# Performance work log

Hardware: AMD Instinct MI355X
Metric: run time of the kernel (lower is better)

The kernel has to match this reference:

```python
import jax, jax.numpy as jnp
from jax import lax
import numpy as np

D_MODEL, D_STATE, D_CONV, D_INNER = 1024, 16, 4, 2048
BATCH, SEQ = 2, 2048


def setup_inputs() -> dict:
    key = jax.random.key(0)
    ks = jax.random.split(key, 7)
    s = lambda fan: 1.0 / np.sqrt(fan)
    return {
        "x": jax.random.normal(ks[0], (BATCH, SEQ, D_MODEL), jnp.float32),
        "W_in": jax.random.normal(ks[1], (2 * D_INNER, D_MODEL), jnp.float32) * s(D_MODEL),
        "conv_w": jax.random.normal(ks[2], (D_INNER, 1, D_CONV), jnp.float32) * s(D_CONV),
        "conv_b": jax.random.normal(ks[3], (D_INNER,), jnp.float32) * 0.02,
        "A_log": jax.random.normal(ks[4], (D_INNER, D_STATE), jnp.float32),
        "W_x": jax.random.normal(ks[5], (2 * D_STATE + 1, D_INNER), jnp.float32) * s(D_INNER),
        "W_out": jax.random.normal(ks[6], (D_MODEL, D_INNER), jnp.float32) * s(D_INNER),
    }


def reference(x, W_in, conv_w, conv_b, A_log, W_x, W_out):
    B, L, _ = x.shape
    di, ds = D_INNER, D_STATE

    # in_proj and chunk into (x_proj, z)
    xz = jnp.einsum("bld,ed->ble", x, W_in)          # [B, L, 2*di]
    xp, z = xz[..., :di], xz[..., di:]

    # depthwise causal conv1d: padding = d_conv-1 on left, then trim to L
    xc = jnp.transpose(xp, (0, 2, 1))                 # [B, di, L]
    xc = lax.conv_general_dilated(
        xc, conv_w, window_strides=(1,), padding=[(D_CONV - 1, 0)],
        feature_group_count=di)
    xc = xc + conv_b[None, :, None]
    xc = jnp.transpose(xc, (0, 2, 1))                 # [B, L, di]
    xc = jax.nn.silu(xc)

    A = -jnp.exp(A_log.astype(jnp.float32))           # [di, ds]

    # input-dependent delta, B, C
    xdbl = jnp.einsum("bld,ed->ble", xc, W_x)         # [B, L, 2*ds+1]
    delta = jax.nn.softplus(xdbl[..., :1])            # [B, L, 1]
    Bm = xdbl[..., 1:1 + ds]                          # [B, L, ds]
    Cm = xdbl[..., 1 + ds:]                           # [B, L, ds]

    # selective scan: h_t = exp(delta_t * A) * h_{t-1} + delta_t * B_t (outer) u_t
    def step(h, inp):
        d_t, b_t, c_t, u_t = inp                      # [B,1], [B,ds], [B,ds], [B,di]
        dA = jnp.exp(d_t[:, :, None] * A[None])       # [B, di, ds]
        h = dA * h + d_t[:, :, None] * b_t[:, None, :] * u_t[:, :, None]
        y_t = jnp.einsum("bds,bs->bd", h, c_t)        # [B, di]
        return h, y_t

    h0 = jnp.zeros((B, di, ds), xc.dtype)
    inps = (jnp.swapaxes(delta, 0, 1), jnp.swapaxes(Bm, 0, 1),
            jnp.swapaxes(Cm, 0, 1), jnp.swapaxes(xc, 0, 1))
    _, ys = lax.scan(step, h0, inps)                  # ys: [L, B, di]
    y = jnp.swapaxes(ys, 0, 1)                        # [B, L, di]

    y = y * jax.nn.silu(z)
    return jnp.einsum("bld,ed->ble", y, W_out)        # [B, L, d_model]
```

## Files before the change

kernel.cpp:

```cpp
#include <hip/hip_runtime.h>

#define DM    1024
#define DS    16
#define DI    2048
#define LSEQ  2048
#define BL    4096
#define NC    128
#define CHK   16

typedef float          f32x4  __attribute__((ext_vector_type(4)));
typedef float          f32x16 __attribute__((ext_vector_type(16)));
typedef unsigned int   u32x4  __attribute__((ext_vector_type(4)));
typedef unsigned short u16x8  __attribute__((ext_vector_type(8)));

__device__ __forceinline__ unsigned short f2bf(float f) {
    unsigned int u = __float_as_uint(f);
    u += 0x7fffu + ((u >> 16) & 1u);
    return (unsigned short)(u >> 16);
}

__device__ __forceinline__ float bf2f(unsigned short u) {
    return __uint_as_float((unsigned int)u << 16);
}

__device__ __forceinline__ float silu_f(float x) {
    return x / (1.f + __expf(-x));
}

__device__ __forceinline__ void mfma_bf16(f32x4& d, const u32x4& a, const u32x4& b) {
    asm("v_mfma_f32_16x16x32_bf16 %0, %1, %2, %0" : "+v"(d) : "v"(a), "v"(b));
}

__device__ __forceinline__ void gload16(const void* g, void* l) {
    __builtin_amdgcn_global_load_lds(
        (const __attribute__((address_space(1))) unsigned int*)g,
        (__attribute__((address_space(3))) unsigned int*)l, 16, 0, 0);
}

__global__ __launch_bounds__(256) void prep_inputs_kernel(const float* __restrict__ x,
                                                          const float* __restrict__ W_in,
                                                          unsigned short* __restrict__ xbf,
                                                          unsigned short* __restrict__ wbf) {
    const int n4 = (BL * DM) / 4;
    int i = blockIdx.x * 256 + threadIdx.x;
    const float* src = (i < n4) ? x : W_in;
    unsigned short* dst = (i < n4) ? xbf : wbf;
    int j = (i < n4) ? i : i - n4;
    float4 v = *(const float4*)(src + j * 4);
    ushort4 o;
    o.x = f2bf(v.x); o.y = f2bf(v.y); o.z = f2bf(v.z); o.w = f2bf(v.w);
    *(ushort4*)(dst + j * 4) = o;
}

__global__ __launch_bounds__(256) void prep_weights_kernel(const float* __restrict__ W_out,
                                                           const float* __restrict__ Wx,
                                                           unsigned short* __restrict__ wobf,
                                                           unsigned short* __restrict__ wxbf) {
    const int n4 = (DM * DI) / 4;
    int i = blockIdx.x * 256 + threadIdx.x;
    if (i < n4) {
        float4 v = *(const float4*)(W_out + i * 4);
        ushort4 o;
        o.x = f2bf(v.x); o.y = f2bf(v.y); o.z = f2bf(v.z); o.w = f2bf(v.w);
        *(ushort4*)(wobf + i * 4) = o;
    } else {
        int j = i - n4;
        if (j < 128 * 2048) {
            int e = j >> 11;
            wxbf[j] = (e < 33) ? f2bf(Wx[j]) : (unsigned short)0;
        }
    }
}

template <typename OUT>
__global__ __launch_bounds__(512, 2) void gemm256_bf16_nt(const unsigned short* __restrict__ A,
                                                          const unsigned short* __restrict__ B,
                                                          OUT* __restrict__ C,
                                                          int M, int N, int K) {
    __shared__ unsigned short As[4][256 * 32];
    __shared__ unsigned short Bs[4][256 * 32];

    const int tid  = threadIdx.x;
    const int lane = tid & 63;
    const int wave = tid >> 6;
    const int wm = wave >> 2;
    const int wn = wave & 3;
    const int lrow = lane & 15, lkh = lane >> 4;
    const int swa  = (lrow >> 1) & 3;

    const long m0 = (long)blockIdx.y * 256;
    const long n0 = (long)blockIdx.x * 256;

    const int scb = ((tid & 3) ^ ((tid >> 3) & 3)) * 8;
    const unsigned short* pa = A + (m0 + (tid >> 2)) * K + scb;
    const unsigned short* pb = B + (n0 + (tid >> 2)) * K + scb;
    const long rstep = (long)128 * K;

    const int NT = K >> 5;

    f32x4 acc[8][4];
#pragma unroll
    for (int i = 0; i < 8; ++i)
#pragma unroll
        for (int j = 0; j < 4; ++j)
            acc[i][j] = (f32x4){0.f, 0.f, 0.f, 0.f};

#define STAGE_A(t) { char* d_ = (char*)&As[(t) & 3][0] + wave * 1024;          \
                     gload16(pa + (long)(t) * 32,         d_);                 \
                     gload16(pa + rstep + (long)(t) * 32, d_ + 8192); }
#define STAGE_B(t) { char* d_ = (char*)&Bs[(t) & 3][0] + wave * 1024;          \
                     gload16(pb + (long)(t) * 32,         d_);                 \
                     gload16(pb + rstep + (long)(t) * 32, d_ + 8192); }

    STAGE_A(0); STAGE_B(0);
    STAGE_A(1); STAGE_B(1);
    STAGE_A(2); STAGE_B(2);
    asm volatile("s_waitcnt vmcnt(8)" ::: "memory");
    __builtin_amdgcn_s_barrier();
    __builtin_amdgcn_sched_barrier(0);

    for (int t = 0; t < NT; ++t) {
        const unsigned short* as = &As[t & 3][0];
        const unsigned short* bs = &Bs[t & 3][0];
        const bool st = (t + 3 < NT);

        u32x4 af[4], bfr[4];
#pragma unroll
        for (int j = 0; j < 4; ++j)
            bfr[j] = *(const u32x4*)(bs + (wn * 64 + j * 16 + lrow) * 32 + ((lkh ^ swa) * 8));
#pragma unroll
        for (int i = 0; i < 4; ++i)
            af[i] = *(const u32x4*)(as + (wm * 128 + i * 16 + lrow) * 32 + ((lkh ^ swa) * 8));
        if (st) STAGE_A(t + 3);
        asm volatile("s_waitcnt lgkmcnt(0)" ::: "memory");
        __builtin_amdgcn_sched_barrier(0);
        __builtin_amdgcn_s_setprio(1);
#pragma unroll
        for (int i = 0; i < 4; ++i)
#pragma unroll
            for (int j = 0; j < 4; ++j)
                mfma_bf16(acc[i][j], af[i], bfr[j]);
        __builtin_amdgcn_s_setprio(0);

#pragma unroll
        for (int i = 0; i < 4; ++i)
            af[i] = *(const u32x4*)(as + (wm * 128 + (i + 4) * 16 + lrow) * 32 + ((lkh ^ swa) * 8));
        if (st) STAGE_B(t + 3);
        asm volatile("s_waitcnt lgkmcnt(0)" ::: "memory");
        __builtin_amdgcn_sched_barrier(0);
        __builtin_amdgcn_s_setprio(1);
#pragma unroll
        for (int i = 0; i < 4; ++i)
#pragma unroll
            for (int j = 0; j < 4; ++j)
                mfma_bf16(acc[i + 4][j], af[i], bfr[j]);
        __builtin_amdgcn_s_setprio(0);

        if (t < NT - 1) {
            if (t <= NT - 4)      asm volatile("s_waitcnt vmcnt(8)" ::: "memory");
            else if (t == NT - 3) asm volatile("s_waitcnt vmcnt(4)" ::: "memory");
            else                  asm volatile("s_waitcnt vmcnt(0)" ::: "memory");
            __builtin_amdgcn_s_barrier();
            __builtin_amdgcn_sched_barrier(0);
        }
    }
#undef STAGE_A
#undef STAGE_B

    asm volatile("s_nop 7\n\ts_nop 7" ::: "memory");

#pragma unroll
    for (int i = 0; i < 8; ++i)
#pragma unroll
        for (int j = 0; j < 4; ++j)
#pragma unroll
            for (int r = 0; r < 4; ++r) {
                long row = m0 + wm * 128 + i * 16 + lkh * 4 + r;
                long col = n0 + wn * 64 + j * 16 + lrow;
                float v = acc[i][j][r];
                if constexpr (sizeof(OUT) == 2) C[row * (long)N + col] = f2bf(v);
                else                            C[row * (long)N + col] = v;
            }
}

template <int NF, typename OUT>
__global__ __launch_bounds__(256) void gemm_bf16_nt(const unsigned short* __restrict__ A,
                                                    const unsigned short* __restrict__ B,
                                                    OUT* __restrict__ C,
                                                    int M, int N, int K, int KS) {
    constexpr int BN = NF * 32;
    __shared__ unsigned short As[2][128 * 32];
    __shared__ unsigned short Bs[2][BN * 32];

    const int tid  = threadIdx.x;
    const int lane = tid & 63;
    const int wave = tid >> 6;
    const int wr = wave >> 1, wc = wave & 1;
    const int lrow = lane & 15, lkh = lane >> 4;

    const long m0 = (long)blockIdx.y * 128;
    const long n0 = (long)blockIdx.x * BN;
    const int koff = blockIdx.z * KS;

    const int scb = ((tid & 3) ^ ((tid >> 3) & 3)) * 8;
    const unsigned short* pa = A + (m0 + (tid >> 2)) * K + koff + scb;
    const unsigned short* pb = B + (n0 + (tid >> 2)) * K + koff + scb;
    const long half = (long)64 * K;

    OUT* Cz = C + (long)blockIdx.z * M * (long)N;

    const int swa = (lrow >> 1) & 3;

    f32x4 acc[4][NF];
#pragma unroll
    for (int i = 0; i < 4; ++i)
#pragma unroll
        for (int j = 0; j < NF; ++j)
            acc[i][j] = (f32x4){0.f, 0.f, 0.f, 0.f};

    auto STAGE = [&](int buf, int k0) {
        char* a = (char*)&As[buf][0] + wave * 1024;
        gload16(pa + k0,        a);
        gload16(pa + half + k0, a + 4096);
        char* b = (char*)&Bs[buf][0] + wave * 1024;
        gload16(pb + k0, b);
        if constexpr (NF == 4) gload16(pb + half + k0, b + 4096);
    };

    STAGE(0, 0);
    asm volatile("s_waitcnt vmcnt(0)" ::: "memory");
    __builtin_amdgcn_s_barrier();
    __builtin_amdgcn_sched_barrier(0);

    int cur = 0;
    for (int k0 = 0; k0 < KS; k0 += 32) {
        const bool notlast = (k0 + 32 < KS);
        if (notlast) STAGE(cur ^ 1, k0 + 32);

        u32x4 af[4], bfr[NF];
#pragma unroll
        for (int i = 0; i < 4; ++i)
            af[i] = *(const u32x4*)(&As[cur][(wr * 64 + i * 16 + lrow) * 32 + ((lkh ^ swa) * 8)]);
#pragma unroll
        for (int j = 0; j < NF; ++j)
            bfr[j] = *(const u32x4*)(&Bs[cur][(wc * NF * 16 + j * 16 + lrow) * 32 + ((lkh ^ swa) * 8)]);

        __builtin_amdgcn_s_setprio(1);
#pragma unroll
        for (int i = 0; i < 4; ++i)
#pragma unroll
            for (int j = 0; j < NF; ++j)
                mfma_bf16(acc[i][j], af[i], bfr[j]);
        __builtin_amdgcn_s_setprio(0);

        if (notlast) {
            asm volatile("s_waitcnt vmcnt(0)" ::: "memory");
            __builtin_amdgcn_s_barrier();
            __builtin_amdgcn_sched_barrier(0);
            cur ^= 1;
        }
    }

    asm volatile("s_nop 7\n\ts_nop 7" ::: "memory");

#pragma unroll
    for (int i = 0; i < 4; ++i)
#pragma unroll
        for (int j = 0; j < NF; ++j)
#pragma unroll
            for (int r = 0; r < 4; ++r) {
                long row = m0 + wr * 64 + i * 16 + lkh * 4 + r;
                long col = n0 + wc * NF * 16 + j * 16 + lrow;
                float v = acc[i][j][r];
                if constexpr (sizeof(OUT) == 2) Cz[row * (long)N + col] = f2bf(v);
                else                            Cz[row * (long)N + col] = v;
            }
}

__global__ __launch_bounds__(256) void conv_silu_kernel(const unsigned short* __restrict__ xzbf,
                                                        const float* __restrict__ cw,
                                                        const float* __restrict__ cb,
                                                        unsigned short* __restrict__ xcbf) {
    int idx = blockIdx.x * 256 + threadIdx.x;
    int d8 = (idx & 255) * 8;
    int m  = idx >> 8;
    int t  = m & (LSEQ - 1);
    const unsigned short* p = xzbf + (long)m * (2 * DI) + d8;
    u16x8 tap0 = (u16x8)(0), tap1 = (u16x8)(0), tap2 = (u16x8)(0);
    u16x8 tap3 = *(const u16x8*)(p);
    if (t >= 1) tap2 = *(const u16x8*)(p - 1 * 2 * DI);
    if (t >= 2) tap1 = *(const u16x8*)(p - 2 * 2 * DI);
    if (t >= 3) tap0 = *(const u16x8*)(p - 3 * 2 * DI);

    u16x8 o;
#pragma unroll
    for (int k = 0; k < 8; ++k) {
        const float4 wv = *(const float4*)(cw + 4 * (d8 + k));
        float s = cb[d8 + k];
        s = fmaf(bf2f(tap0[k]), wv.x, s);
        s = fmaf(bf2f(tap1[k]), wv.y, s);
        s = fmaf(bf2f(tap2[k]), wv.z, s);
        s = fmaf(bf2f(tap3[k]), wv.w, s);
        o[k] = f2bf(silu_f(s));
    }
    *(u16x8*)(xcbf + (long)m * DI + d8) = o;
}

__global__ __launch_bounds__(256) void xdbl_reduce_kernel(const float* __restrict__ part,
                                                          float* __restrict__ dlt,
                                                          float* __restrict__ BC) {
    int idx = blockIdx.x * 256 + threadIdx.x;
    if (idx >= BL * 33) return;
    int m = idx / 33;
    int j = idx - m * 33;
    float v = 0.f;
#pragma unroll
    for (int g = 0; g < 8; ++g) v += part[(long)g * (BL * 128) + (long)m * 128 + j];
    if (j == 0) dlt[m] = (v > 20.f) ? v : log1pf(expf(v));
    else        BC[(long)m * 32 + (j - 1)] = v;
}

__global__ __launch_bounds__(256, 4) void scan_pass1(const float* __restrict__ dlt,
                                                     const float* __restrict__ BC,
                                                     const unsigned short* __restrict__ xcbf,
                                                     const float* __restrict__ A_log,
                                                     float* __restrict__ P_,
                                                     float* __restrict__ S_) {
    __shared__ float sdl[CHK];
    __shared__ float sbc[CHK * 32];

    const int tid = threadIdx.x;
    const int c   = blockIdx.x;
    const int ch  = blockIdx.y * 256 + tid;
    const int b   = ch >> 11;
    const int d   = ch & (DI - 1);
    const long m0 = (long)b * LSEQ + (long)c * CHK;

    if (tid < CHK * 8) *(float4*)(sbc + tid * 4) = *(const float4*)(BC + m0 * 32 + tid * 4);
    if (tid < CHK) sdl[tid] = dlt[m0 + tid];

    f32x16 A2, h;
#pragma unroll
    for (int s = 0; s < 16; ++s) {
        A2[s] = -__expf(A_log[d * 16 + s]) * 1.44269504f;
        h[s] = 0.f;
    }
    const unsigned short* ur = xcbf + m0 * DI + d;
    float sumdl = 0.f;
    __syncthreads();

#pragma unroll
    for (int t0 = 0; t0 < CHK; t0 += 4) {
        float uu[4], dd[4];
#pragma unroll
        for (int k = 0; k < 4; ++k) {
            uu[k] = bf2f(ur[(long)(t0 + k) * DI]);
            dd[k] = sdl[t0 + k];
        }
#pragma unroll
        for (int k = 0; k < 4; ++k) {
            const int t = t0 + k;
            float dl = dd[k];
            float du = dl * uu[k];
            sumdl += dl;
#pragma unroll
            for (int q = 0; q < 4; ++q) {
                f32x4 bq = *(const f32x4*)(sbc + t * 32 + q * 4);
#pragma unroll
                for (int j = 0; j < 4; ++j) {
                    const int s = q * 4 + j;
                    float dA = exp2f(dl * A2[s]);
                    h[s] = fmaf(dA, h[s], du * bq[j]);
                }
            }
        }
    }
    float* pp = P_ + ((long)c * 4096 + ch) * 16;
    float* sp = S_ + ((long)c * 4096 + ch) * 16;
#pragma unroll
    for (int q = 0; q < 4; ++q) {
        f32x4 pv;
#pragma unroll
        for (int j = 0; j < 4; ++j) pv[j] = exp2f(A2[q * 4 + j] * sumdl);
        *(f32x4*)(pp + q * 4) = pv;
        *(f32x4*)(sp + q * 4) = (f32x4){h[q*4], h[q*4+1], h[q*4+2], h[q*4+3]};
    }
}

__global__ __launch_bounds__(256) void scan_pass2(const float* __restrict__ P_,
                                                  float* __restrict__ S_) {
    const long idx = (long)blockIdx.x * 256 + threadIdx.x;
    float h = 0.f;
    for (int c0 = 0; c0 < NC; c0 += 8) {
        float p[8], s[8];
#pragma unroll
        for (int i = 0; i < 8; ++i) {
            p[i] = P_[(long)(c0 + i) * 65536 + idx];
            s[i] = S_[(long)(c0 + i) * 65536 + idx];
        }
#pragma unroll
        for (int i = 0; i < 8; ++i) {
            S_[(long)(c0 + i) * 65536 + idx] = h;
            h = fmaf(p[i], h, s[i]);
        }
    }
}

__global__ __launch_bounds__(256, 4) void scan_pass3(const float* __restrict__ dlt,
                                                     const float* __restrict__ BC,
                                                     const unsigned short* __restrict__ xcbf,
                                                     const unsigned short* __restrict__ xzbf,
                                                     const float* __restrict__ A_log,
                                                     const float* __restrict__ H0,
                                                     unsigned short* __restrict__ ybf) {
    __shared__ float sdl[CHK];
    __shared__ float sbc[CHK * 32];

    const int tid = threadIdx.x;
    const int c   = blockIdx.x;
    const int ch  = blockIdx.y * 256 + tid;
    const int b   = ch >> 11;
    const int d   = ch & (DI - 1);
    const long m0 = (long)b * LSEQ + (long)c * CHK;

    if (tid < CHK * 8) *(float4*)(sbc + tid * 4) = *(const float4*)(BC + m0 * 32 + tid * 4);
    if (tid < CHK) sdl[tid] = dlt[m0 + tid];

    f32x16 A2, h;
    const float* h0p = H0 + ((long)c * 4096 + ch) * 16;
    {
        f32x4 h0a = *(const f32x4*)(h0p + 0);
        f32x4 h0b = *(const f32x4*)(h0p + 4);
        f32x4 h0c = *(const f32x4*)(h0p + 8);
        f32x4 h0d = *(const f32x4*)(h0p + 12);
#pragma unroll
        for (int j = 0; j < 4; ++j) {
            h[j]      = h0a[j];
            h[4 + j]  = h0b[j];
            h[8 + j]  = h0c[j];
            h[12 + j] = h0d[j];
        }
    }
#pragma unroll
    for (int s = 0; s < 16; ++s) A2[s] = -__expf(A_log[d * 16 + s]) * 1.44269504f;

    const unsigned short* ur = xcbf + m0 * DI + d;
    const unsigned short* zr = xzbf + m0 * (2 * DI) + DI + d;
    unsigned short* yr = ybf + m0 * DI + d;
    __syncthreads();

#pragma unroll
    for (int t0 = 0; t0 < CHK; t0 += 4) {
        float uu[4], zz[4], dd[4];
#pragma unroll
        for (int k = 0; k < 4; ++k) {
            uu[k] = bf2f(ur[(long)(t0 + k) * DI]);
            zz[k] = bf2f(zr[(long)(t0 + k) * 2 * DI]);
            dd[k] = sdl[t0 + k];
        }
#pragma unroll
        for (int k = 0; k < 4; ++k) {
            const int t = t0 + k;
            float dl = dd[k];
            float du = dl * uu[k];
            f32x4 yv = (f32x4){0.f, 0.f, 0.f, 0.f};
#pragma unroll
            for (int q = 0; q < 4; ++q) {
                f32x4 bq = *(const f32x4*)(sbc + t * 32 + q * 4);
                f32x4 cq = *(const f32x4*)(sbc + t * 32 + 16 + q * 4);
#pragma unroll
                for (int j = 0; j < 4; ++j) {
                    const int s = q * 4 + j;
                    float dA = exp2f(dl * A2[s]);
                    h[s] = fmaf(dA, h[s], du * bq[j]);
                    yv[q] = fmaf(h[s], cq[j], yv[q]);
                }
            }
            float y = (yv[0] + yv[1]) + (yv[2] + yv[3]);
            yr[(long)t * DI] = f2bf(y * silu_f(zz[k]));
        }
    }
}

extern "C" void kernel_launch(void* const* d_in, const int* in_sizes, int n_in,
                              void* d_out, int out_size, void* d_ws, size_t ws_size,
                              hipStream_t stream) {
    const float* x      = (const float*)d_in[0];
    const float* W_in   = (const float*)d_in[1];
    const float* conv_w = (const float*)d_in[2];
    const float* conv_b = (const float*)d_in[3];
    const float* A_log  = (const float*)d_in[4];
    const float* W_x    = (const float*)d_in[5];
    const float* W_out  = (const float*)d_in[6];
    float* out = (float*)d_out;

    char* w = (char*)d_ws;
    unsigned short* xbf  = (unsigned short*)(w + 0);
    unsigned short* wbf  = (unsigned short*)(w + 8388608);
    unsigned short* xzbf = (unsigned short*)(w + 16777216);
    unsigned short* xcbf = (unsigned short*)(w + 50331648);
    float*          dlt  = (float*)(w + 67108864);
    float*          BC   = (float*)(w + 67125248);
    float*          P_   = (float*)(w + 67649536);
    float*          S_   = (float*)(w + 101203968);

    unsigned short* wobf      = xbf;
    unsigned short* wxbf      = (unsigned short*)(w + 8388608);
    float*          xdbl_part = (float*)P_;
    unsigned short* ybf       = (unsigned short*)P_;

    prep_inputs_kernel<<<dim3(8192), dim3(256), 0, stream>>>(x, W_in, xbf, wbf);
    gemm256_bf16_nt<unsigned short><<<dim3(16, 16), dim3(512), 0, stream>>>(xbf, wbf, xzbf, BL, 2 * DI, DM);
    prep_weights_kernel<<<dim3(3072), dim3(256), 0, stream>>>(W_out, W_x, wobf, wxbf);
    conv_silu_kernel<<<dim3((BL * DI / 8) / 256), dim3(256), 0, stream>>>(xzbf, conv_w, conv_b, xcbf);
    gemm_bf16_nt<4, float><<<dim3(1, 32, 8), dim3(256), 0, stream>>>(xcbf, wxbf, xdbl_part, BL, 128, DI, 256);
    xdbl_reduce_kernel<<<dim3(528), dim3(256), 0, stream>>>(xdbl_part, dlt, BC);
    scan_pass1<<<dim3(NC, 16), dim3(256), 0, stream>>>(dlt, BC, xcbf, A_log, P_, S_);
    scan_pass2<<<dim3(256), dim3(256), 0, stream>>>(P_, S_);
    scan_pass3<<<dim3(NC, 16), dim3(256), 0, stream>>>(dlt, BC, xcbf, xzbf, A_log, S_, ybf);
    gemm_bf16_nt<2, float><<<dim3(16, 32, 1), dim3(256), 0, stream>>>(ybf, wobf, out, BL, DM, DI, DI);
}
```

Before: 229.6 us.

## Precompute A2 in prep kernel, double scan chunk size, drop scan LDS staging

```diff
diff --git a/kernel.cpp b/kernel.cpp
--- a/kernel.cpp
+++ b/kernel.cpp
@@ -5,13 +5,19 @@
 #define DI    2048
 #define LSEQ  2048
 #define BL    4096
-#define NC    128
-#define CHK   16
+#define NC    64
+#define CHK   32
 
 typedef float          f32x4  __attribute__((ext_vector_type(4)));
 typedef float          f32x16 __attribute__((ext_vector_type(16)));
 typedef unsigned int   u32x4  __attribute__((ext_vector_type(4)));
 typedef unsigned short u16x8  __attribute__((ext_vector_type(8)));
+
+#if __has_builtin(__builtin_amdgcn_exp2f)
+#define EXP2(x) __builtin_amdgcn_exp2f(x)
+#else
+#define EXP2(x) __expf((x) * 0.6931471805599453f)
+#endif
 
 __device__ __forceinline__ unsigned short f2bf(float f) {
     unsigned int u = __float_as_uint(f);
@@ -54,8 +60,10 @@
 
 __global__ __launch_bounds__(256) void prep_weights_kernel(const float* __restrict__ W_out,
                                                            const float* __restrict__ Wx,
+                                                           const float* __restrict__ A_log,
                                                            unsigned short* __restrict__ wobf,
-                                                           unsigned short* __restrict__ wxbf) {
+                                                           unsigned short* __restrict__ wxbf,
+                                                           float* __restrict__ A2) {
     const int n4 = (DM * DI) / 4;
     int i = blockIdx.x * 256 + threadIdx.x;
     if (i < n4) {
@@ -68,6 +76,9 @@
         if (j < 128 * 2048) {
             int e = j >> 11;
             wxbf[j] = (e < 33) ? f2bf(Wx[j]) : (unsigned short)0;
+        } else {
+            int k = j - 128 * 2048;
+            if (k < DI * DS) A2[k] = -__expf(A_log[k]) * 1.44269504f;
         }
     }
 }
@@ -320,15 +331,12 @@
     else        BC[(long)m * 32 + (j - 1)] = v;
 }
 
-__global__ __launch_bounds__(256, 4) void scan_pass1(const float* __restrict__ dlt,
-                                                     const float* __restrict__ BC,
-                                                     const unsigned short* __restrict__ xcbf,
-                                                     const float* __restrict__ A_log,
-                                                     float* __restrict__ P_,
-                                                     float* __restrict__ S_) {
-    __shared__ float sdl[CHK];
-    __shared__ float sbc[CHK * 32];
-
+__global__ __launch_bounds__(256) void scan_pass1(const float* __restrict__ dlt,
+                                                  const float* __restrict__ BC,
+                                                  const unsigned short* __restrict__ xcbf,
+                                                  const float* __restrict__ A2t,
+                                                  float* __restrict__ P_,
+                                                  float* __restrict__ S_) {
     const int tid = threadIdx.x;
     const int c   = blockIdx.x;
     const int ch  = blockIdx.y * 256 + tid;
@@ -336,40 +344,42 @@
     const int d   = ch & (DI - 1);
     const long m0 = (long)b * LSEQ + (long)c * CHK;
 
-    if (tid < CHK * 8) *(float4*)(sbc + tid * 4) = *(const float4*)(BC + m0 * 32 + tid * 4);
-    if (tid < CHK) sdl[tid] = dlt[m0 + tid];
-
     f32x16 A2, h;
-#pragma unroll
-    for (int s = 0; s < 16; ++s) {
-        A2[s] = -__expf(A_log[d * 16 + s]) * 1.44269504f;
-        h[s] = 0.f;
+    {
+        const float* ap = A2t + d * 16;
+        f32x4 a0 = *(const f32x4*)(ap + 0);
+        f32x4 a1 = *(const f32x4*)(ap + 4);
+        f32x4 a2 = *(const f32x4*)(ap + 8);
+        f32x4 a3 = *(const f32x4*)(ap + 12);
+#pragma unroll
+        for (int j = 0; j < 4; ++j) {
+            A2[j] = a0[j]; A2[4 + j] = a1[j]; A2[8 + j] = a2[j]; A2[12 + j] = a3[j];
+            h[j] = 0.f; h[4 + j] = 0.f; h[8 + j] = 0.f; h[12 + j] = 0.f;
+        }
     }
     const unsigned short* ur = xcbf + m0 * DI + d;
+    const float* br = BC + m0 * 32;
+    const float* dr = dlt + m0;
     float sumdl = 0.f;
-    __syncthreads();
 
 #pragma unroll
     for (int t0 = 0; t0 < CHK; t0 += 4) {
-        float uu[4], dd[4];
-#pragma unroll
-        for (int k = 0; k < 4; ++k) {
-            uu[k] = bf2f(ur[(long)(t0 + k) * DI]);
-            dd[k] = sdl[t0 + k];
-        }
+        float uu[4];
+#pragma unroll
+        for (int k = 0; k < 4; ++k) uu[k] = bf2f(ur[(long)(t0 + k) * DI]);
 #pragma unroll
         for (int k = 0; k < 4; ++k) {
             const int t = t0 + k;
-            float dl = dd[k];
+            float dl = dr[t];
             float du = dl * uu[k];
             sumdl += dl;
 #pragma unroll
             for (int q = 0; q < 4; ++q) {
-                f32x4 bq = *(const f32x4*)(sbc + t * 32 + q * 4);
+                f32x4 bq = *(const f32x4*)(br + t * 32 + q * 4);
 #pragma unroll
                 for (int j = 0; j < 4; ++j) {
                     const int s = q * 4 + j;
-                    float dA = exp2f(dl * A2[s]);
+                    float dA = EXP2(dl * A2[s]);
                     h[s] = fmaf(dA, h[s], du * bq[j]);
                 }
             }
@@ -381,7 +391,7 @@
     for (int q = 0; q < 4; ++q) {
         f32x4 pv;
 #pragma unroll
-        for (int j = 0; j < 4; ++j) pv[j] = exp2f(A2[q * 4 + j] * sumdl);
+        for (int j = 0; j < 4; ++j) pv[j] = EXP2(A2[q * 4 + j] * sumdl);
         *(f32x4*)(pp + q * 4) = pv;
         *(f32x4*)(sp + q * 4) = (f32x4){h[q*4], h[q*4+1], h[q*4+2], h[q*4+3]};
     }
@@ -406,16 +416,13 @@
     }
 }
 
-__global__ __launch_bounds__(256, 4) void scan_pass3(const float* __restrict__ dlt,
-                                                     const float* __restrict__ BC,
-                                                     const unsigned short* __restrict__ xcbf,
-                                                     const unsigned short* __restrict__ xzbf,
-                                                     const float* __restrict__ A_log,
-                                                     const float* __restrict__ H0,
-                                                     unsigned short* __restrict__ ybf) {
-    __shared__ float sdl[CHK];
-    __shared__ float sbc[CHK * 32];
-
+__global__ __launch_bounds__(256) void scan_pass3(const float* __restrict__ dlt,
+                                                  const float* __restrict__ BC,
+                                                  const unsigned short* __restrict__ xcbf,
+                                                  const unsigned short* __restrict__ xzbf,
+                                                  const float* __restrict__ A2t,
+                                                  const float* __restrict__ H0,
+                                                  unsigned short* __restrict__ ybf) {
     const int tid = threadIdx.x;
     const int c   = blockIdx.x;
     const int ch  = blockIdx.y * 256 + tid;
@@ -423,55 +430,53 @@
     const int d   = ch & (DI - 1);
     const long m0 = (long)b * LSEQ + (long)c * CHK;
 
-    if (tid < CHK * 8) *(float4*)(sbc + tid * 4) = *(const float4*)(BC + m0 * 32 + tid * 4);
-    if (tid < CHK) sdl[tid] = dlt[m0 + tid];
-
     f32x16 A2, h;
-    const float* h0p = H0 + ((long)c * 4096 + ch) * 16;
     {
+        const float* ap = A2t + d * 16;
+        f32x4 a0 = *(const f32x4*)(ap + 0);
+        f32x4 a1 = *(const f32x4*)(ap + 4);
+        f32x4 a2 = *(const f32x4*)(ap + 8);
+        f32x4 a3 = *(const f32x4*)(ap + 12);
+        const float* h0p = H0 + ((long)c * 4096 + ch) * 16;
         f32x4 h0a = *(const f32x4*)(h0p + 0);
         f32x4 h0b = *(const f32x4*)(h0p + 4);
         f32x4 h0c = *(const f32x4*)(h0p + 8);
         f32x4 h0d = *(const f32x4*)(h0p + 12);
 #pragma unroll
         for (int j = 0; j < 4; ++j) {
-            h[j]      = h0a[j];
-            h[4 + j]  = h0b[j];
-            h[8 + j]  = h0c[j];
-            h[12 + j] = h0d[j];
-        }
-    }
-#pragma unroll
-    for (int s = 0; s < 16; ++s) A2[s] = -__expf(A_log[d * 16 + s]) * 1.44269504f;
+            A2[j] = a0[j]; A2[4 + j] = a1[j]; A2[8 + j] = a2[j]; A2[12 + j] = a3[j];
+            h[j] = h0a[j]; h[4 + j] = h0b[j]; h[8 + j] = h0c[j]; h[12 + j] = h0d[j];
+        }
+    }
 
     const unsigned short* ur = xcbf + m0 * DI + d;
     const unsigned short* zr = xzbf + m0 * (2 * DI) + DI + d;
+    const float* br = BC + m0 * 32;
+    const float* dr = dlt + m0;
     unsigned short* yr = ybf + m0 * DI + d;
-    __syncthreads();
 
 #pragma unroll
     for (int t0 = 0; t0 < CHK; t0 += 4) {
-        float uu[4], zz[4], dd[4];
+        float uu[4], zz[4];
 #pragma unroll
         for (int k = 0; k < 4; ++k) {
             uu[k] = bf2f(ur[(long)(t0 + k) * DI]);
             zz[k] = bf2f(zr[(long)(t0 + k) * 2 * DI]);
-            dd[k] = sdl[t0 + k];
         }
 #pragma unroll
         for (int k = 0; k < 4; ++k) {
             const int t = t0 + k;
-            float dl = dd[k];
+            float dl = dr[t];
             float du = dl * uu[k];
             f32x4 yv = (f32x4){0.f, 0.f, 0.f, 0.f};
 #pragma unroll
             for (int q = 0; q < 4; ++q) {
-                f32x4 bq = *(const f32x4*)(sbc + t * 32 + q * 4);
-                f32x4 cq = *(const f32x4*)(sbc + t * 32 + 16 + q * 4);
+                f32x4 bq = *(const f32x4*)(br + t * 32 + q * 4);
+                f32x4 cq = *(const f32x4*)(br + t * 32 + 16 + q * 4);
 #pragma unroll
                 for (int j = 0; j < 4; ++j) {
                     const int s = q * 4 + j;
-                    float dA = exp2f(dl * A2[s]);
+                    float dA = EXP2(dl * A2[s]);
                     h[s] = fmaf(dA, h[s], du * bq[j]);
                     yv[q] = fmaf(h[s], cq[j], yv[q]);
                 }
@@ -502,7 +507,8 @@
     float*          dlt  = (float*)(w + 67108864);
     float*          BC   = (float*)(w + 67125248);
     float*          P_   = (float*)(w + 67649536);
-    float*          S_   = (float*)(w + 101203968);
+    float*          S_   = (float*)(w + 84426752);
+    float*          A2   = (float*)(w + 101203968);
 
     unsigned short* wobf      = xbf;
     unsigned short* wxbf      = (unsigned short*)(w + 8388608);
@@ -511,12 +517,12 @@
 
     prep_inputs_kernel<<<dim3(8192), dim3(256), 0, stream>>>(x, W_in, xbf, wbf);
     gemm256_bf16_nt<unsigned short><<<dim3(16, 16), dim3(512), 0, stream>>>(xbf, wbf, xzbf, BL, 2 * DI, DM);
-    prep_weights_kernel<<<dim3(3072), dim3(256), 0, stream>>>(W_out, W_x, wobf, wxbf);
+    prep_weights_kernel<<<dim3(3200), dim3(256), 0, stream>>>(W_out, W_x, A_log, wobf, wxbf, A2);
     conv_silu_kernel<<<dim3((BL * DI / 8) / 256), dim3(256), 0, stream>>>(xzbf, conv_w, conv_b, xcbf);
     gemm_bf16_nt<4, float><<<dim3(1, 32, 8), dim3(256), 0, stream>>>(xcbf, wxbf, xdbl_part, BL, 128, DI, 256);
     xdbl_reduce_kernel<<<dim3(528), dim3(256), 0, stream>>>(xdbl_part, dlt, BC);
-    scan_pass1<<<dim3(NC, 16), dim3(256), 0, stream>>>(dlt, BC, xcbf, A_log, P_, S_);
+    scan_pass1<<<dim3(NC, 16), dim3(256), 0, stream>>>(dlt, BC, xcbf, A2, P_, S_);
     scan_pass2<<<dim3(256), dim3(256), 0, stream>>>(P_, S_);
-    scan_pass3<<<dim3(NC, 16), dim3(256), 0, stream>>>(dlt, BC, xcbf, xzbf, A_log, S_, ybf);
+    scan_pass3<<<dim3(NC, 16), dim3(256), 0, stream>>>(dlt, BC, xcbf, xzbf, A2, S_, ybf);
     gemm_bf16_nt<2, float><<<dim3(16, 32, 1), dim3(256), 0, stream>>>(ybf, wobf, out, BL, DM, DI, DI);
 }
```

Measured after the change: 209.1 us. 8.9% less time.
